# Kernel tuning notes

Hardware: AMD Instinct MI355X
Metric: run time of the kernel (lower is better)

## Reference

```python
import jax, jax.numpy as jnp
import numpy as np

NUM_ENT = 7
DIM_ENT = 4
NEMBED_HALF = 128  # nembed_ctx / 2
BATCH = 16384


def setup_inputs() -> dict:
    key = jax.random.key(0)
    k1, k2, k3, k4, k5 = jax.random.split(key, 5)
    ctx = jax.random.normal(k1, (NUM_ENT * DIM_ENT, BATCH), dtype=jnp.float32)
    init = 0.01
    w_prop = jax.random.uniform(k2, (DIM_ENT, NEMBED_HALF), jnp.float32, -init, init)
    b_prop = jax.random.uniform(k3, (NEMBED_HALF,), jnp.float32, -init, init)
    w_rel = jax.random.uniform(k4, (DIM_ENT + 1, NEMBED_HALF), jnp.float32, -init, init)
    b_rel = jax.random.uniform(k5, (NEMBED_HALF,), jnp.float32, -init, init)
    return {"ctx": ctx, "w_prop": w_prop, "b_prop": b_prop, "w_rel": w_rel, "b_rel": b_rel}


def reference(ctx, w_prop, b_prop, w_rel, b_rel):
    # ctx: [num_ent*dim_ent, B] -> ents: [B, num_ent, dim_ent]
    ents = ctx.T.reshape(-1, NUM_ENT, DIM_ENT)
    # property embedding: Linear + ReLU (dropout = identity at inference)
    prop_emb = jax.nn.relu(jnp.einsum('bnd,dh->bnh', ents, w_prop) + b_prop)
    # pairwise diffs [B, i, j, d] and euclidean distance over first two coords
    diffs = ents[:, :, None, :] - ents[:, None, :, :]
    dist = jnp.sqrt(diffs[..., 0] ** 2 + diffs[..., 1] ** 2)  # [B, i, j]
    feats = jnp.concatenate([diffs, dist[..., None]], axis=-1)  # [B, i, j, dim_ent+1]
    rel = jax.nn.relu(jnp.einsum('bijd,dh->bijh', feats, w_rel) + b_rel)
    # original loops skip i == j: zero the diagonal before summing over j
    off_diag = (1.0 - jnp.eye(NUM_ENT, dtype=rel.dtype))[None, :, :, None]
    rel_emb = jnp.sum(rel * off_diag, axis=2)  # [B, num_ent, H]
    return jnp.concatenate([prop_emb, rel_emb], axis=2)  # [B, num_ent, 2H]
```

## Files before the change

kernel.cpp:

```cpp
#include <hip/hip_runtime.h>

#define NUM_ENT 7
#define DIM_ENT 4
#define H 128
#define OUTC (2 * H)
#define B_PER_BLOCK 4

__global__ __launch_bounds__(256) void ace_kernel(
    const float* __restrict__ ctx,
    const float* __restrict__ w_prop,
    const float* __restrict__ b_prop,
    const float* __restrict__ w_rel,
    const float* __restrict__ b_rel,
    float* __restrict__ out,
    int B)
{
    __shared__ float s_ents[B_PER_BLOCK][NUM_ENT * DIM_ENT];
    __shared__ float s_feat[B_PER_BLOCK][NUM_ENT][NUM_ENT][5];

    const int tid = threadIdx.x;
    const int b0 = blockIdx.x * B_PER_BLOCK;

    if (tid < B_PER_BLOCK * NUM_ENT * DIM_ENT) {
        const int bb = tid / (NUM_ENT * DIM_ENT);
        const int k  = tid % (NUM_ENT * DIM_ENT);
        s_ents[bb][k] = ctx[(size_t)k * B + (b0 + bb)];
    }
    __syncthreads();

    if (tid < B_PER_BLOCK * NUM_ENT * NUM_ENT) {
        const int bb = tid / (NUM_ENT * NUM_ENT);
        const int p  = tid % (NUM_ENT * NUM_ENT);
        const int i  = p / NUM_ENT;
        const int j  = p % NUM_ENT;
        const float dx = s_ents[bb][i * 4 + 0] - s_ents[bb][j * 4 + 0];
        const float dy = s_ents[bb][i * 4 + 1] - s_ents[bb][j * 4 + 1];
        const float dz = s_ents[bb][i * 4 + 2] - s_ents[bb][j * 4 + 2];
        const float dw = s_ents[bb][i * 4 + 3] - s_ents[bb][j * 4 + 3];
        s_feat[bb][i][j][0] = dx;
        s_feat[bb][i][j][1] = dy;
        s_feat[bb][i][j][2] = dz;
        s_feat[bb][i][j][3] = dw;
        s_feat[bb][i][j][4] = sqrtf(dx * dx + dy * dy);
    }
    __syncthreads();

    const int bb   = tid >> 6;
    const int lane = tid & 63;
    const int b    = b0 + bb;
    float* outb = out + (size_t)b * (NUM_ENT * OUTC);
    const int c = lane * 4;

    if (lane < 32) {
        const float4 w0 = *(const float4*)(w_prop + 0 * H + c);
        const float4 w1 = *(const float4*)(w_prop + 1 * H + c);
        const float4 w2 = *(const float4*)(w_prop + 2 * H + c);
        const float4 w3 = *(const float4*)(w_prop + 3 * H + c);
        const float4 bp = *(const float4*)(b_prop + c);
#pragma unroll
        for (int n = 0; n < NUM_ENT; ++n) {
            const float e0 = s_ents[bb][n * 4 + 0];
            const float e1 = s_ents[bb][n * 4 + 1];
            const float e2 = s_ents[bb][n * 4 + 2];
            const float e3 = s_ents[bb][n * 4 + 3];
            float4 a;
            a.x = fmaxf(bp.x + e0 * w0.x + e1 * w1.x + e2 * w2.x + e3 * w3.x, 0.f);
            a.y = fmaxf(bp.y + e0 * w0.y + e1 * w1.y + e2 * w2.y + e3 * w3.y, 0.f);
            a.z = fmaxf(bp.z + e0 * w0.z + e1 * w1.z + e2 * w2.z + e3 * w3.z, 0.f);
            a.w = fmaxf(bp.w + e0 * w0.w + e1 * w1.w + e2 * w2.w + e3 * w3.w, 0.f);
            *(float4*)(outb + n * OUTC + c) = a;
        }
    } else {
        const int h = c - H;
        const float4 w0 = *(const float4*)(w_rel + 0 * H + h);
        const float4 w1 = *(const float4*)(w_rel + 1 * H + h);
        const float4 w2 = *(const float4*)(w_rel + 2 * H + h);
        const float4 w3 = *(const float4*)(w_rel + 3 * H + h);
        const float4 w4 = *(const float4*)(w_rel + 4 * H + h);
        const float4 br = *(const float4*)(b_rel + h);
#pragma unroll
        for (int i = 0; i < NUM_ENT; ++i) {
            float4 acc = {0.f, 0.f, 0.f, 0.f};
#pragma unroll
            for (int j = 0; j < NUM_ENT; ++j) {
                if (j == i) continue;
                const float f0 = s_feat[bb][i][j][0];
                const float f1 = s_feat[bb][i][j][1];
                const float f2 = s_feat[bb][i][j][2];
                const float f3 = s_feat[bb][i][j][3];
                const float f4 = s_feat[bb][i][j][4];
                acc.x += fmaxf(br.x + f0 * w0.x + f1 * w1.x + f2 * w2.x + f3 * w3.x + f4 * w4.x, 0.f);
                acc.y += fmaxf(br.y + f0 * w0.y + f1 * w1.y + f2 * w2.y + f3 * w3.y + f4 * w4.y, 0.f);
                acc.z += fmaxf(br.z + f0 * w0.z + f1 * w1.z + f2 * w2.z + f3 * w3.z + f4 * w4.z, 0.f);
                acc.w += fmaxf(br.w + f0 * w0.w + f1 * w1.w + f2 * w2.w + f3 * w3.w + f4 * w4.w, 0.f);
            }
            *(float4*)(outb + i * OUTC + c) = acc;
        }
    }
}

extern "C" void kernel_launch(void* const* d_in, const int* in_sizes, int n_in,
                              void* d_out, int out_size, void* d_ws, size_t ws_size,
                              hipStream_t stream) {
    const float* ctx    = (const float*)d_in[0];
    const float* w_prop = (const float*)d_in[1];
    const float* b_prop = (const float*)d_in[2];
    const float* w_rel  = (const float*)d_in[3];
    const float* b_rel  = (const float*)d_in[4];
    float* out = (float*)d_out;

    const int B = in_sizes[0] / (NUM_ENT * DIM_ENT);
    const int grid = (B + B_PER_BLOCK - 1) / B_PER_BLOCK;
    ace_kernel<<<grid, 256, 0, stream>>>(ctx, w_prop, b_prop, w_rel, b_rel, out, B);
}
```

Before: 152.5 us.

## Split prop and rel work into separate blocks to remove wave divergence

The grid now holds twice as many blocks: the first half compute only the relational embedding and the second half only the property embedding, each for 8 batch items per block. Before, each wave split its lanes between the cheap prop branch and the heavy rel branch, so the two branches ran serially and half the lanes sat idle in each. Now every wave runs one path uniformly, and the prop blocks skip the pairwise-feature stage and its barrier. The cost is that ctx entries are loaded twice, once by each block type, and the two block types carry very different amounts of work.

```diff
diff --git a/kernel.cpp b/kernel.cpp
--- a/kernel.cpp
+++ b/kernel.cpp
@@ -4,7 +4,7 @@
 #define DIM_ENT 4
 #define H 128
 #define OUTC (2 * H)
-#define B_PER_BLOCK 4
+#define BPB 8
 
 __global__ __launch_bounds__(256) void ace_kernel(
     const float* __restrict__ ctx,
@@ -15,69 +15,54 @@
     float* __restrict__ out,
     int B)
 {
-    __shared__ float s_ents[B_PER_BLOCK][NUM_ENT * DIM_ENT];
-    __shared__ float s_feat[B_PER_BLOCK][NUM_ENT][NUM_ENT][5];
+    __shared__ float s_ents[BPB][NUM_ENT * DIM_ENT];
+    __shared__ float s_feat[BPB][NUM_ENT][NUM_ENT][5];
 
     const int tid = threadIdx.x;
-    const int b0 = blockIdx.x * B_PER_BLOCK;
+    const int nb = gridDim.x >> 1;
+    const bool is_rel = blockIdx.x < nb;
+    const int blk = is_rel ? blockIdx.x : (blockIdx.x - nb);
+    const int b0 = blk * BPB;
 
-    if (tid < B_PER_BLOCK * NUM_ENT * DIM_ENT) {
-        const int bb = tid / (NUM_ENT * DIM_ENT);
-        const int k  = tid % (NUM_ENT * DIM_ENT);
+    if (tid < BPB * NUM_ENT * DIM_ENT) {
+        const int k  = tid >> 3;
+        const int bb = tid & 7;
         s_ents[bb][k] = ctx[(size_t)k * B + (b0 + bb)];
     }
     __syncthreads();
 
-    if (tid < B_PER_BLOCK * NUM_ENT * NUM_ENT) {
-        const int bb = tid / (NUM_ENT * NUM_ENT);
-        const int p  = tid % (NUM_ENT * NUM_ENT);
-        const int i  = p / NUM_ENT;
-        const int j  = p % NUM_ENT;
-        const float dx = s_ents[bb][i * 4 + 0] - s_ents[bb][j * 4 + 0];
-        const float dy = s_ents[bb][i * 4 + 1] - s_ents[bb][j * 4 + 1];
-        const float dz = s_ents[bb][i * 4 + 2] - s_ents[bb][j * 4 + 2];
-        const float dw = s_ents[bb][i * 4 + 3] - s_ents[bb][j * 4 + 3];
-        s_feat[bb][i][j][0] = dx;
-        s_feat[bb][i][j][1] = dy;
-        s_feat[bb][i][j][2] = dz;
-        s_feat[bb][i][j][3] = dw;
-        s_feat[bb][i][j][4] = sqrtf(dx * dx + dy * dy);
+    if (is_rel) {
+        for (int t = tid; t < BPB * NUM_ENT * NUM_ENT; t += 256) {
+            const int bb = t / (NUM_ENT * NUM_ENT);
+            const int p  = t % (NUM_ENT * NUM_ENT);
+            const int i  = p / NUM_ENT;
+            const int j  = p % NUM_ENT;
+            const float dx = s_ents[bb][i * 4 + 0] - s_ents[bb][j * 4 + 0];
+            const float dy = s_ents[bb][i * 4 + 1] - s_ents[bb][j * 4 + 1];
+            const float dz = s_ents[bb][i * 4 + 2] - s_ents[bb][j * 4 + 2];
+            const float dw = s_ents[bb][i * 4 + 3] - s_ents[bb][j * 4 + 3];
+            s_feat[bb][i][j][0] = dx;
+            s_feat[bb][i][j][1] = dy;
+            s_feat[bb][i][j][2] = dz;
+            s_feat[bb][i][j][3] = dw;
+            s_feat[bb][i][j][4] = sqrtf(dx * dx + dy * dy);
+        }
+        __syncthreads();
     }
-    __syncthreads();
 
-    const int bb   = tid >> 6;
+    const int w    = tid >> 6;
     const int lane = tid & 63;
-    const int b    = b0 + bb;
-    float* outb = out + (size_t)b * (NUM_ENT * OUTC);
-    const int c = lane * 4;
+    const int bb   = w * 2 + (lane >> 5);
+    const int c4   = (lane & 31) << 2;
+    float* outb = out + (size_t)(b0 + bb) * (NUM_ENT * OUTC);
 
-    if (lane < 32) {
-        const float4 w0 = *(const float4*)(w_prop + 0 * H + c);
-        const float4 w1 = *(const float4*)(w_prop + 1 * H + c);
-        const float4 w2 = *(const float4*)(w_prop + 2 * H + c);
-        const float4 w3 = *(const float4*)(w_prop + 3 * H + c);
-        const float4 bp = *(const float4*)(b_prop + c);
-#pragma unroll
-        for (int n = 0; n < NUM_ENT; ++n) {
-            const float e0 = s_ents[bb][n * 4 + 0];
-            const float e1 = s_ents[bb][n * 4 + 1];
-            const float e2 = s_ents[bb][n * 4 + 2];
-            const float e3 = s_ents[bb][n * 4 + 3];
-            float4 a;
-            a.x = fmaxf(bp.x + e0 * w0.x + e1 * w1.x + e2 * w2.x + e3 * w3.x, 0.f);
-            a.y = fmaxf(bp.y + e0 * w0.y + e1 * w1.y + e2 * w2.y + e3 * w3.y, 0.f);
-            a.z = fmaxf(bp.z + e0 * w0.z + e1 * w1.z + e2 * w2.z + e3 * w3.z, 0.f);
-            a.w = fmaxf(bp.w + e0 * w0.w + e1 * w1.w + e2 * w2.w + e3 * w3.w, 0.f);
-            *(float4*)(outb + n * OUTC + c) = a;
-        }
-    } else {
-        const int h = c - H;
-        const float4 w0 = *(const float4*)(w_rel + 0 * H + h);
-        const float4 w1 = *(const float4*)(w_rel + 1 * H + h);
-        const float4 w2 = *(const float4*)(w_rel + 2 * H + h);
-        const float4 w3 = *(const float4*)(w_rel + 3 * H + h);
-        const float4 w4 = *(const float4*)(w_rel + 4 * H + h);
-        const float4 br = *(const float4*)(b_rel + h);
+    if (is_rel) {
+        const float4 w0 = *(const float4*)(w_rel + 0 * H + c4);
+        const float4 w1 = *(const float4*)(w_rel + 1 * H + c4);
+        const float4 w2 = *(const float4*)(w_rel + 2 * H + c4);
+        const float4 w3 = *(const float4*)(w_rel + 3 * H + c4);
+        const float4 w4 = *(const float4*)(w_rel + 4 * H + c4);
+        const float4 br = *(const float4*)(b_rel + c4);
 #pragma unroll
         for (int i = 0; i < NUM_ENT; ++i) {
             float4 acc = {0.f, 0.f, 0.f, 0.f};
@@ -94,7 +79,26 @@
                 acc.z += fmaxf(br.z + f0 * w0.z + f1 * w1.z + f2 * w2.z + f3 * w3.z + f4 * w4.z, 0.f);
                 acc.w += fmaxf(br.w + f0 * w0.w + f1 * w1.w + f2 * w2.w + f3 * w3.w + f4 * w4.w, 0.f);
             }
-            *(float4*)(outb + i * OUTC + c) = acc;
+            *(float4*)(outb + i * OUTC + H + c4) = acc;
+        }
+    } else {
+        const float4 w0 = *(const float4*)(w_prop + 0 * H + c4);
+        const float4 w1 = *(const float4*)(w_prop + 1 * H + c4);
+        const float4 w2 = *(const float4*)(w_prop + 2 * H + c4);
+        const float4 w3 = *(const float4*)(w_prop + 3 * H + c4);
+        const float4 bp = *(const float4*)(b_prop + c4);
+#pragma unroll
+        for (int n = 0; n < NUM_ENT; ++n) {
+            const float e0 = s_ents[bb][n * 4 + 0];
+            const float e1 = s_ents[bb][n * 4 + 1];
+            const float e2 = s_ents[bb][n * 4 + 2];
+            const float e3 = s_ents[bb][n * 4 + 3];
+            float4 a;
+            a.x = fmaxf(bp.x + e0 * w0.x + e1 * w1.x + e2 * w2.x + e3 * w3.x, 0.f);
+            a.y = fmaxf(bp.y + e0 * w0.y + e1 * w1.y + e2 * w2.y + e3 * w3.y, 0.f);
+            a.z = fmaxf(bp.z + e0 * w0.z + e1 * w1.z + e2 * w2.z + e3 * w3.z, 0.f);
+            a.w = fmaxf(bp.w + e0 * w0.w + e1 * w1.w + e2 * w2.w + e3 * w3.w, 0.f);
+            *(float4*)(outb + n * OUTC + c4) = a;
         }
     }
 }
@@ -110,6 +114,6 @@
     float* out = (float*)d_out;
 
     const int B = in_sizes[0] / (NUM_ENT * DIM_ENT);
-    const int grid = (B + B_PER_BLOCK - 1) / B_PER_BLOCK;
-    ace_kernel<<<grid, 256, 0, stream>>>(ctx, w_prop, b_prop, w_rel, b_rel, out, B);
+    const int nb = (B + BPB - 1) / BPB;
+    ace_kernel<<<2 * nb, 256, 0, stream>>>(ctx, w_prop, b_prop, w_rel, b_rel, out, B);
 }
```

Result: faster. 135.2 us (median of 2 runs) (-11.3%).
